# Kernel tuning notes

Hardware: AMD Instinct MI355X
Metric: run time of the kernel (lower is better)

## Reference

```python
import jax, jax.numpy as jnp
import numpy as np

N = 50000
E = 800000
IN_C = 128
OUT_C = 64   # per-head dim C == out_channels (concat=False)
HEADS = 4
FFN_H = 256
SQRT_HALF = 0.70710678
LN_EPS = 1e-7


def setup_inputs() -> dict:
    key = jax.random.key(0)
    ks = jax.random.split(key, 16)
    s = 0.05
    return {
        "x": jax.random.normal(ks[0], (N, IN_C), jnp.float32),
        "edge_index": jax.random.randint(ks[1], (2, E), 0, N, jnp.int64),
        # GATv2 params
        "Wl": jax.random.normal(ks[2], (HEADS * OUT_C, IN_C), jnp.float32) * s,
        "Wr": jax.random.normal(ks[3], (HEADS * OUT_C, IN_C), jnp.float32) * s,
        "att": jax.random.normal(ks[4], (HEADS, OUT_C), jnp.float32) * s,
        "bias": jax.random.normal(ks[5], (OUT_C,), jnp.float32) * s,
        # block linears
        "W_affn1": jax.random.normal(ks[6], (OUT_C, IN_C), jnp.float32) * s,
        "b_affn1": jnp.zeros((OUT_C,), jnp.float32),
        "W_affn2": jax.random.normal(ks[7], (OUT_C, OUT_C), jnp.float32) * s,
        "b_affn2": jnp.zeros((OUT_C,), jnp.float32),
        # layernorms
        "g1": jnp.ones((IN_C,), jnp.float32),
        "beta1": jnp.zeros((IN_C,), jnp.float32),
        "g2": jnp.ones((OUT_C,), jnp.float32),
        "beta2": jnp.zeros((OUT_C,), jnp.float32),
        # FFN: out_channels -> 256 -> out_channels
        "W1": jax.random.normal(ks[8], (FFN_H, OUT_C), jnp.float32) * s,
        "b1": jnp.zeros((FFN_H,), jnp.float32),
        "W2": jax.random.normal(ks[9], (OUT_C, FFN_H), jnp.float32) * s,
        "b2": jnp.zeros((OUT_C,), jnp.float32),
    }


def _ln(v, g, b):
    m = jnp.mean(v, axis=-1, keepdims=True)
    var = jnp.var(v, axis=-1, keepdims=True)
    return (v - m) * jax.lax.rsqrt(var + LN_EPS) * g + b


def reference(x, edge_index, Wl, Wr, att, bias, W_affn1, b_affn1,
              W_affn2, b_affn2, g1, beta1, g2, beta2, W1, b1, W2, b2):
    n = x.shape[0]
    H, C = att.shape
    dst = edge_index[0]
    src = edge_index[1]

    x_res = x @ W_affn1.T + b_affn1            # (N, OUT_C)
    h = _ln(x, g1, beta1)                      # (N, IN_C)

    # GATv2 attention (concat=False, no self loops)
    x_l = (h @ Wl.T).reshape(n, H, C)
    x_r = (h @ Wr.T).reshape(n, H, C)
    x_j = x_r[src]                             # (E, H, C)
    e = jax.nn.leaky_relu(x_l[dst] + x_j, 0.2) # (E, H, C)
    logits = jnp.einsum('ehc,hc->eh', e, att)  # (E, H)

    # segment softmax over destination nodes (per head)
    mx = jax.ops.segment_max(logits, dst, num_segments=n)
    ex = jnp.exp(logits - mx[dst])
    den = jax.ops.segment_sum(ex, dst, num_segments=n)
    alpha = ex / (den[dst] + 1e-16)            # (E, H)

    agg = jnp.zeros((n, H, C), x.dtype).at[dst].add(x_j * alpha[..., None])
    attn_out = jnp.mean(agg, axis=1) + bias    # (N, OUT_C)

    out = SQRT_HALF * attn_out + SQRT_HALF * x_res

    # FFN half of the block (pre-LN, matching the attention half's structure)
    h2 = _ln(out, g2, beta2)
    f = jax.nn.relu(h2 @ W1.T + b1) @ W2.T + b2
    res2 = out @ W_affn2.T + b_affn2
    return SQRT_HALF * f + SQRT_HALF * res2
```

## Files before the change

kernel.cpp:

```cpp
#include <hip/hip_runtime.h>
#include <hip/hip_bf16.h>
#include <hip/hip_fp16.h>
#include <math.h>


#define SQRT_HALF 0.70710678f
#define LN_EPS 1e-7f

typedef __attribute__((ext_vector_type(8))) short bf16x8;
typedef __attribute__((ext_vector_type(4))) float f32x4;
typedef _Float16 f16x2 __attribute__((ext_vector_type(2)));

__device__ __forceinline__ float wave_reduce_sum64(float v) {
  #pragma unroll
  for (int m = 1; m < 64; m <<= 1) v += __shfl_xor(v, m, 64);
  return v;
}
__device__ __forceinline__ unsigned short f2bf_bits(float f) {
  __hip_bfloat16 b = __float2bfloat16(f);
  return *reinterpret_cast<unsigned short*>(&b);
}
__device__ __forceinline__ unsigned int pack2bf(float lo, float hi) {
  return (unsigned int)f2bf_bits(lo) | ((unsigned int)f2bf_bits(hi) << 16);
}
__device__ __forceinline__ __half2 u2h(unsigned int u) {
  union { unsigned int u; __half2 h; } c; c.u = u; return c.h;
}
__device__ __forceinline__ __half2 h2abs(__half2 v) {
  union { __half2 h; unsigned int u; } c; c.h = v;
  c.u &= 0x7fff7fffu;
  return c.h;
}
__device__ __forceinline__ f16x2 h2f(__half2 h) {
  union { __half2 h; f16x2 f; } c; c.h = h; return c.f;
}
__device__ __forceinline__ __half2 shflx_h2(__half2 v, int m) {
  union { unsigned int u; __half2 h; } c; c.h = v;
  c.u = (unsigned int)__shfl_xor((int)c.u, m, 64);
  return c.h;
}
__device__ __forceinline__ float dpp_xor1_add(float p) {
  int t = __builtin_amdgcn_update_dpp(0, __float_as_int(p), 0xB1, 0xf, 0xf, true);
  return p + __int_as_float(t);
}
__device__ __forceinline__ float dpp_xor2_add(float p) {
  int t = __builtin_amdgcn_update_dpp(0, __float_as_int(p), 0x4E, 0xf, 0xf, true);
  return p + __int_as_float(t);
}

__global__ __launch_bounds__(256) void phase0(
    const float* __restrict__ x, const float* __restrict__ g1,
    const float* __restrict__ beta1, __hip_bfloat16* __restrict__ h,
    __hip_bfloat16* __restrict__ xbf,
    const float* __restrict__ wl, const float* __restrict__ wr,
    const float* __restrict__ wa1, const float* __restrict__ w1,
    const float* __restrict__ w2, const float* __restrict__ wa2,
    const float* __restrict__ b2c, const float* __restrict__ ba2,
    const float* __restrict__ att,
    __hip_bfloat16* __restrict__ wcat, __hip_bfloat16* __restrict__ wa1b,
    __hip_bfloat16* __restrict__ w1b, __hip_bfloat16* __restrict__ w2b,
    __hip_bfloat16* __restrict__ wa2b, __half* __restrict__ att2,
    float* __restrict__ biasc,
    const int* __restrict__ ei, int* __restrict__ cursorE,
    unsigned short* __restrict__ ell,
    int E_, int n, int gLN, int gW) {
  int bx = blockIdx.x;
  if (bx < gLN) {
    int node = bx * 4 + (threadIdx.x >> 6);
    if (node >= n) return;
    int lane = threadIdx.x & 63;
    const float* xr = x + (size_t)node * 128;
    float a = xr[lane], c = xr[lane + 64];
    float s1 = wave_reduce_sum64(a + c) * (1.f / 128.f);
    float s2 = wave_reduce_sum64(a * a + c * c) * (1.f / 128.f);
    float inv = rsqrtf(s2 - s1 * s1 + LN_EPS);
    __hip_bfloat16* hr = h + (size_t)node * 128;
    hr[lane]      = __float2bfloat16((a - s1) * inv * g1[lane] + beta1[lane]);
    hr[lane + 64] =
        __float2bfloat16((c - s1) * inv * g1[lane + 64] + beta1[lane + 64]);
    __hip_bfloat16* xbr = xbf + (size_t)node * 128;
    xbr[lane]      = __float2bfloat16(a);
    xbr[lane + 64] = __float2bfloat16(c);
  } else if (bx < gLN + gW) {
    int i = (bx - gLN) * 256 + threadIdx.x;
    if (i < 65536) {
      wcat[i] = __float2bfloat16(i < 32768 ? wl[i] : wr[i - 32768]);
    } else if (i < 73728) {
      int j = i - 65536; wa1b[j] = __float2bfloat16(wa1[j]);
    } else if (i < 90112) {
      int j = i - 73728; w1b[j] = __float2bfloat16(w1[j]);
    } else if (i < 106496) {
      int j = i - 90112; w2b[j] = __float2bfloat16(w2[j]);
    } else if (i < 110592) {
      int j = i - 106496; wa2b[j] = __float2bfloat16(wa2[j]);
    } else if (i < 110848) {
      int j = i - 110592; att2[j] = __float2half(att[j]);
    } else if (i < 110912) {
      int j = i - 110848; biasc[j] = SQRT_HALF * (b2c[j] + ba2[j]);
    }
  } else {
    int e = (bx - gLN - gW) * 256 + threadIdx.x;
    if (e < E_) {
      int dst = ei[e], src = ei[E_ + e];
      int pos = atomicAdd(&cursorE[dst << 4], 1);
      if (pos < 64) ell[((size_t)dst << 6) + pos] = (unsigned short)src;
    }
  }
}

__global__ __launch_bounds__(256) void mfma_pre(
    const short* __restrict__ h, const short* __restrict__ xbf,
    const short* __restrict__ wcat, const short* __restrict__ wa1b,
    const float* __restrict__ ba1, __half* __restrict__ xlxr,
    float* __restrict__ xres, int n, int ntiles) {
  int tid = threadIdx.x;
  int wv = tid >> 6, l = tid & 63;
  int lane_m = l & 15, kg = l >> 4;
  if (blockIdx.y < 4) {
    int bn = blockIdx.y * 128;
    bf16x8 wf[4][8];
    const short* wp = wcat + (size_t)(bn + lane_m) * 128 + kg * 8;
    #pragma unroll
    for (int ks = 0; ks < 4; ++ks)
      #pragma unroll
      for (int ct = 0; ct < 8; ++ct)
        wf[ks][ct] = *(const bf16x8*)(wp + (size_t)ct * 16 * 128 + ks * 32);
    for (int t = blockIdx.x; t < ntiles; t += gridDim.x) {
      int node = t * 64 + wv * 16 + lane_m;
      int nodec = node < n ? node : n - 1;
      const short* ap = h + (size_t)nodec * 128 + kg * 8;
      f32x4 acc[8] = {};
      #pragma unroll
      for (int ks = 0; ks < 4; ++ks) {
        bf16x8 af = *(const bf16x8*)(ap + ks * 32);
        #pragma unroll
        for (int ct = 0; ct < 8; ++ct)
          acc[ct] = __builtin_amdgcn_mfma_f32_16x16x32_bf16(
              wf[ks][ct], af, acc[ct], 0, 0, 0);
      }
      if (node < n) {
        #pragma unroll
        for (int ct = 0; ct < 8; ++ct) {
          int col = bn + ct * 16 + kg * 4;
          ushort4 s;
          s.x = __half_as_ushort(__float2half(acc[ct][0]));
          s.y = __half_as_ushort(__float2half(acc[ct][1]));
          s.z = __half_as_ushort(__float2half(acc[ct][2]));
          s.w = __half_as_ushort(__float2half(acc[ct][3]));
          *(ushort4*)((unsigned short*)xlxr + (size_t)node * 512 + col) = s;
        }
      }
    }
  } else {
    bf16x8 wf[4][4];
    const short* wp = wa1b + (size_t)lane_m * 128 + kg * 8;
    #pragma unroll
    for (int ks = 0; ks < 4; ++ks)
      #pragma unroll
      for (int ct = 0; ct < 4; ++ct)
        wf[ks][ct] = *(const bf16x8*)(wp + (size_t)ct * 16 * 128 + ks * 32);
    float4 bias4[4];
    #pragma unroll
    for (int ct = 0; ct < 4; ++ct)
      bias4[ct] = *(const float4*)(ba1 + ct * 16 + kg * 4);
    for (int t = blockIdx.x; t < ntiles; t += gridDim.x) {
      int node = t * 64 + wv * 16 + lane_m;
      int nodec = node < n ? node : n - 1;
      const short* ap = xbf + (size_t)nodec * 128 + kg * 8;
      f32x4 acc[4] = {};
      #pragma unroll
      for (int ks = 0; ks < 4; ++ks) {
        bf16x8 af = *(const bf16x8*)(ap + ks * 32);
        #pragma unroll
        for (int ct = 0; ct < 4; ++ct)
          acc[ct] = __builtin_amdgcn_mfma_f32_16x16x32_bf16(
              wf[ks][ct], af, acc[ct], 0, 0, 0);
      }
      if (node < n) {
        #pragma unroll
        for (int ct = 0; ct < 4; ++ct) {
          int col = ct * 16 + kg * 4;
          *(float4*)(xres + (size_t)node * 64 + col) = make_float4(
              acc[ct][0] + ((const float*)&bias4[ct])[0],
              acc[ct][1] + ((const float*)&bias4[ct])[1],
              acc[ct][2] + ((const float*)&bias4[ct])[2],
              acc[ct][3] + ((const float*)&bias4[ct])[3]);
        }
      }
    }
  }
}

__global__ __launch_bounds__(256) void fused_edge_kernel(
    const int* __restrict__ cursorE, const unsigned short* __restrict__ ell,
    const __half* __restrict__ xlxr,
    const __half* __restrict__ att2, const float* __restrict__ xres,
    const float* __restrict__ bias, const float* __restrict__ g2,
    const float* __restrict__ b2, __hip_bfloat16* __restrict__ outb,
    __hip_bfloat16* __restrict__ h2, int n) {
  int node = blockIdx.x * 4 + (threadIdx.x >> 6);
  if (node >= n) return;
  int lane = threadIdx.x & 63;
  int half_ = lane >> 5;
  int hl = lane & 31;
  int q = hl & 7;
  int off8 = (hl >> 3) * 64 + q * 8;
  uint4 va = *(const uint4*)(xlxr + (size_t)node * 512 + off8);
  __half2 xa2[4] = {u2h(va.x), u2h(va.y), u2h(va.z), u2h(va.w)};
  uint4 vt = *(const uint4*)(att2 + off8);
  const __half2 c06 = __float2half2_rn(0.6f);
  const __half2 c04 = __float2half2_rn(0.4f);
  __half2 at6[4], at4[4];
  #pragma unroll
  for (int c = 0; c < 4; ++c) {
    __half2 a = u2h(((const unsigned int*)&vt)[c]);
    at6[c] = __hmul2(c06, a);
    at4[c] = __hmul2(c04, a);
  }
  int d = cursorE[node << 4];
  d = d < 64 ? d : 64;
  float den = 0.f;
  __half2 ac2[4] = {__float2half2_rn(0.f), __float2half2_rn(0.f),
                    __float2half2_rn(0.f), __float2half2_rn(0.f)};
  if (d > 0) {
    int dm1 = d - 1;
    int dpairs = d >> 1;
    const __half* xrbase = xlxr + 256 + off8;
    int myidx = (int)ell[((size_t)node << 6) + (lane <= dm1 ? lane : dm1)];
    int srcA = __shfl(myidx, half_ <= dm1 ? half_ : dm1, 64);
    int srcB = __shfl(myidx, 2 + half_ <= dm1 ? 2 + half_ : dm1, 64);
    uint4 vbA = *(const uint4*)(xrbase + (size_t)srcA * 512);
    uint4 vbB = *(const uint4*)(xrbase + (size_t)srcB * 512);
    #pragma unroll 2
    for (int k = 0; k < dpairs; ++k) {
      int jC = 2 * k + 4 + half_;
      jC = jC <= dm1 ? jC : dm1;
      int srcC = __shfl(myidx, jC, 64);
      uint4 vbC = *(const uint4*)(xrbase + (size_t)srcC * 512);
      __half2 xb2[4] = {u2h(vbA.x), u2h(vbA.y), u2h(vbA.z), u2h(vbA.w)};
      float p = 0.f;
      #pragma unroll
      for (int c = 0; c < 4; ++c) {
        __half2 s = __hadd2(xa2[c], xb2[c]);
        p = __builtin_amdgcn_fdot2(h2f(at6[c]), h2f(s), p, false);
        p = __builtin_amdgcn_fdot2(h2f(at4[c]), h2f(h2abs(s)), p, false);
      }
      p = dpp_xor1_add(p);
      p = dpp_xor2_add(p);
      p += __shfl_xor(p, 4, 64);
      float ex = __expf(p);
      den += ex;
      __half2 ex2 = __float2half2_rn(ex);
      #pragma unroll
      for (int c = 0; c < 4; ++c) ac2[c] = __hfma2(ex2, xb2[c], ac2[c]);
      vbA = vbB; vbB = vbC;
    }
    if (d & 1) {
      __half2 xb2[4] = {u2h(vbA.x), u2h(vbA.y), u2h(vbA.z), u2h(vbA.w)};
      float p = 0.f;
      #pragma unroll
      for (int c = 0; c < 4; ++c) {
        __half2 s = __hadd2(xa2[c], xb2[c]);
        p = __builtin_amdgcn_fdot2(h2f(at6[c]), h2f(s), p, false);
        p = __builtin_amdgcn_fdot2(h2f(at4[c]), h2f(h2abs(s)), p, false);
      }
      p = dpp_xor1_add(p);
      p = dpp_xor2_add(p);
      p += __shfl_xor(p, 4, 64);
      float ex = (half_ == 0) ? __expf(p) : 0.f;
      den += ex;
      __half2 ex2 = __float2half2_rn(ex);
      #pragma unroll
      for (int c = 0; c < 4; ++c) ac2[c] = __hfma2(ex2, xb2[c], ac2[c]);
    }
  }
  #pragma unroll
  for (int c = 0; c < 4; ++c) ac2[c] = __hadd2(ac2[c], shflx_h2(ac2[c], 32));
  den += __shfl_xor(den, 32, 64);
  float inv = 1.f / (den + 1e-16f);
  __half2 inv2 = __float2half2_rn(inv);
  #pragma unroll
  for (int c = 0; c < 4; ++c) {
    __half2 a = __hmul2(ac2[c], inv2);
    a = __hadd2(a, shflx_h2(a, 8));
    a = __hadd2(a, shflx_h2(a, 16));
    ac2[c] = a;
  }
  float acf[8];
  #pragma unroll
  for (int c = 0; c < 4; ++c) {
    acf[2 * c]     = __low2float(ac2[c]);
    acf[2 * c + 1] = __high2float(ac2[c]);
  }
  float o[8];
  {
    float4 bi0 = *(const float4*)(bias + q * 8);
    float4 bi1 = *(const float4*)(bias + q * 8 + 4);
    float4 xr0 = *(const float4*)(xres + (size_t)node * 64 + q * 8);
    float4 xr1 = *(const float4*)(xres + (size_t)node * 64 + q * 8 + 4);
    float bi[8] = {bi0.x, bi0.y, bi0.z, bi0.w, bi1.x, bi1.y, bi1.z, bi1.w};
    float xr[8] = {xr0.x, xr0.y, xr0.z, xr0.w, xr1.x, xr1.y, xr1.z, xr1.w};
    #pragma unroll
    for (int c = 0; c < 8; ++c)
      o[c] = SQRT_HALF * (acf[c] * 0.25f + bi[c] + xr[c]);
  }
  float s1 = 0.f, s2 = 0.f;
  #pragma unroll
  for (int c = 0; c < 8; ++c) { s1 += o[c]; s2 += o[c] * o[c]; }
  s1 = dpp_xor1_add(s1); s2 = dpp_xor1_add(s2);
  s1 = dpp_xor2_add(s1); s2 = dpp_xor2_add(s2);
  s1 += __shfl_xor(s1, 4, 64); s2 += __shfl_xor(s2, 4, 64);
  float mean = s1 * (1.f / 64.f);
  float var = s2 * (1.f / 64.f) - mean * mean;
  float rinv = rsqrtf(var + LN_EPS);
  if (lane < 8) {
    float4 g0 = *(const float4*)(g2 + q * 8);
    float4 g1v = *(const float4*)(g2 + q * 8 + 4);
    float4 e0 = *(const float4*)(b2 + q * 8);
    float4 e1 = *(const float4*)(b2 + q * 8 + 4);
    float gg[8] = {g0.x, g0.y, g0.z, g0.w, g1v.x, g1v.y, g1v.z, g1v.w};
    float ee[8] = {e0.x, e0.y, e0.z, e0.w, e1.x, e1.y, e1.z, e1.w};
    uint4 ov, hv;
    ov.x = pack2bf(o[0], o[1]); ov.y = pack2bf(o[2], o[3]);
    ov.z = pack2bf(o[4], o[5]); ov.w = pack2bf(o[6], o[7]);
    float t[8];
    #pragma unroll
    for (int c = 0; c < 8; ++c)
      t[c] = (o[c] - mean) * rinv * gg[c] + ee[c];
    hv.x = pack2bf(t[0], t[1]); hv.y = pack2bf(t[2], t[3]);
    hv.z = pack2bf(t[4], t[5]); hv.w = pack2bf(t[6], t[7]);
    *(uint4*)((unsigned short*)outb + (size_t)node * 64 + q * 8) = ov;
    *(uint4*)((unsigned short*)h2 + (size_t)node * 64 + q * 8) = hv;
  }
}

__global__ __launch_bounds__(256) void ffn_fused(
    const __hip_bfloat16* __restrict__ h2, const __hip_bfloat16* __restrict__ outb,
    const __hip_bfloat16* __restrict__ w1b, const __hip_bfloat16* __restrict__ w2b,
    const __hip_bfloat16* __restrict__ wa2b, const float* __restrict__ b1,
    const float* __restrict__ biasc, float* __restrict__ out,
    int n, int ntiles) {
  __shared__ unsigned short lds[4][16][280];
  int tid = threadIdx.x;
  int wv = tid >> 6, l = tid & 63;
  int lane_m = l & 15, kg = l >> 4;
  bf16x8 wf1[2][16];
  #pragma unroll
  for (int ks = 0; ks < 2; ++ks)
    #pragma unroll
    for (int ct = 0; ct < 16; ++ct)
      wf1[ks][ct] = *(const bf16x8*)(
          (const short*)w1b + (size_t)(ct * 16 + lane_m) * 64 + ks * 32 + kg * 8);
  for (int t = blockIdx.x; t < ntiles; t += gridDim.x) {
    int node = t * 64 + wv * 16 + lane_m;
    int nodec = node < n ? node : n - 1;
    const short* hp = (const short*)h2 + (size_t)nodec * 64 + kg * 8;
    bf16x8 af1[2];
    af1[0] = *(const bf16x8*)(hp);
    af1[1] = *(const bf16x8*)(hp + 32);
    f32x4 acc1[16] = {};
    #pragma unroll
    for (int ks = 0; ks < 2; ++ks)
      #pragma unroll
      for (int ct = 0; ct < 16; ++ct)
        acc1[ct] = __builtin_amdgcn_mfma_f32_16x16x32_bf16(
            wf1[ks][ct], af1[ks], acc1[ct], 0, 0, 0);
    #pragma unroll
    for (int ct = 0; ct < 16; ++ct) {
      float4 bb = *(const float4*)(b1 + ct * 16 + kg * 4);
      ushort4 s;
      s.x = f2bf_bits(fmaxf(acc1[ct][0] + bb.x, 0.f));
      s.y = f2bf_bits(fmaxf(acc1[ct][1] + bb.y, 0.f));
      s.z = f2bf_bits(fmaxf(acc1[ct][2] + bb.z, 0.f));
      s.w = f2bf_bits(fmaxf(acc1[ct][3] + bb.w, 0.f));
      *(ushort4*)&lds[wv][lane_m][ct * 16 + kg * 4] = s;
    }
    f32x4 acc2[4] = {};
    #pragma unroll
    for (int ks = 0; ks < 8; ++ks) {
      bf16x8 af2 = *(const bf16x8*)&lds[wv][lane_m][ks * 32 + kg * 8];
      #pragma unroll
      for (int ct = 0; ct < 4; ++ct) {
        bf16x8 wf2 = *(const bf16x8*)(
            (const short*)w2b + (size_t)(ct * 16 + lane_m) * 256 + ks * 32 + kg * 8);
        acc2[ct] = __builtin_amdgcn_mfma_f32_16x16x32_bf16(
            wf2, af2, acc2[ct], 0, 0, 0);
      }
    }
    const short* op = (const short*)outb + (size_t)nodec * 64 + kg * 8;
    #pragma unroll
    for (int ks = 0; ks < 2; ++ks) {
      bf16x8 afo = *(const bf16x8*)(op + ks * 32);
      #pragma unroll
      for (int ct = 0; ct < 4; ++ct) {
        bf16x8 wfo = *(const bf16x8*)(
            (const short*)wa2b + (size_t)(ct * 16 + lane_m) * 64 + ks * 32 + kg * 8);
        acc2[ct] = __builtin_amdgcn_mfma_f32_16x16x32_bf16(
            wfo, afo, acc2[ct], 0, 0, 0);
      }
    }
    if (node < n) {
      #pragma unroll
      for (int ct = 0; ct < 4; ++ct) {
        float4 bc = *(const float4*)(biasc + ct * 16 + kg * 4);
        float4 v = make_float4(SQRT_HALF * acc2[ct][0] + bc.x,
                               SQRT_HALF * acc2[ct][1] + bc.y,
                               SQRT_HALF * acc2[ct][2] + bc.z,
                               SQRT_HALF * acc2[ct][3] + bc.w);
        *(float4*)(out + (size_t)node * 64 + ct * 16 + kg * 4) = v;
      }
    }
  }
}

extern "C" void kernel_launch(void* const* d_in, const int* in_sizes, int n_in,
                              void* d_out, int out_size, void* d_ws,
                              size_t ws_size, hipStream_t stream) {
  const float* x       = (const float*)d_in[0];
  const int*   ei      = (const int*)d_in[1];
  const float* Wl      = (const float*)d_in[2];
  const float* Wr      = (const float*)d_in[3];
  const float* att     = (const float*)d_in[4];
  const float* bias    = (const float*)d_in[5];
  const float* W_affn1 = (const float*)d_in[6];
  const float* b_affn1 = (const float*)d_in[7];
  const float* W_affn2 = (const float*)d_in[8];
  const float* b_affn2 = (const float*)d_in[9];
  const float* g1      = (const float*)d_in[10];
  const float* beta1   = (const float*)d_in[11];
  const float* g2      = (const float*)d_in[12];
  const float* beta2   = (const float*)d_in[13];
  const float* W1      = (const float*)d_in[14];
  const float* b1      = (const float*)d_in[15];
  const float* W2      = (const float*)d_in[16];
  const float* b2      = (const float*)d_in[17];
  int n  = in_sizes[0] / 128;
  int E_ = in_sizes[1] / 2;

  float* ws = (float*)d_ws;
  size_t o_xlxr = 0;
  size_t o_h    = o_xlxr + (size_t)n * 256;
  size_t o_xbf  = o_h + (size_t)n * 64;
  size_t o_xres = o_xbf + (size_t)n * 64;
  size_t o_h2   = o_xres + (size_t)n * 64;
  size_t o_outb = o_h2 + (size_t)n * 32;
  size_t o_w    = o_outb + (size_t)n * 32;
  __half* xlxr         = (__half*)(ws + o_xlxr);
  __hip_bfloat16* h    = (__hip_bfloat16*)(ws + o_h);
  __hip_bfloat16* xbf  = (__hip_bfloat16*)(ws + o_xbf);
  float* xres          = ws + o_xres;
  __hip_bfloat16* h2   = (__hip_bfloat16*)(ws + o_h2);
  __hip_bfloat16* outb = (__hip_bfloat16*)(ws + o_outb);
  __hip_bfloat16* wcat = (__hip_bfloat16*)(ws + o_w);
  __hip_bfloat16* wa1b = (__hip_bfloat16*)(ws + o_w + 32768);
  __hip_bfloat16* w1b  = (__hip_bfloat16*)(ws + o_w + 36864);
  __hip_bfloat16* w2b  = (__hip_bfloat16*)(ws + o_w + 45056);
  __hip_bfloat16* wa2b = (__hip_bfloat16*)(ws + o_w + 53248);
  __half* att2         = (__half*)(ws + o_w + 55296);
  float* biasc         = ws + o_w + 55424;
  size_t o_int = o_w + 55488;
  int* iw        = (int*)(ws + o_int);
  int* cursorE   = iw;
  unsigned short* ell =
      (unsigned short*)(iw + (size_t)n * 16);

  int ntiles = (n + 63) / 64;
  int gLN = (n + 3) / 4;
  int gW = (110912 + 255) / 256;
  int gH = (E_ + 255) / 256;

  (void)hipMemsetAsync(cursorE, 0, (size_t)n * 16 * 4, stream);

  phase0<<<gLN + gW + gH, 256, 0, stream>>>(
      x, g1, beta1, h, xbf, Wl, Wr, W_affn1, W1, W2, W_affn2, b2, b_affn2,
      att, wcat, wa1b, w1b, w2b, wa2b, att2, biasc, ei, cursorE, ell,
      E_, n, gLN, gW);

  mfma_pre<<<dim3(128, 5), 256, 0, stream>>>(
      (const short*)h, (const short*)xbf, (const short*)wcat,
      (const short*)wa1b, b_affn1, xlxr, xres, n, ntiles);

  fused_edge_kernel<<<(n + 3) / 4, 256, 0, stream>>>(
      cursorE, ell, xlxr, att2, xres, bias, g2, beta2, outb, h2, n);

  ffn_fused<<<ntiles, 256, 0, stream>>>(
      h2, outb, w1b, w2b, wa2b, b1, biasc, (float*)d_out, n, ntiles);
}
```

Baseline: 219.8 us.

## Move edge bucketing into GEMM kernel with split front/back cursors

Drops the memset and zeroes the per-node cursors inside phase0. The ELL bucketing of edges moves into a sixth y-slice of mfma_pre, so the scatter overlaps the projection GEMMs, with a 4-way unrolled grid-stride loop. Odd and even threads use two separate cursor arrays, filling slots from the front and from the back, which halves atomic contention per destination. The edge kernel merges the two counts and maps slot indices. The cost is extra cursor memory and per-lane index remapping. Overflow beyond 64 neighbours is now split differently between the two halves.

```diff
diff --git a/kernel.cpp b/kernel.cpp
--- a/kernel.cpp
+++ b/kernel.cpp
@@ -61,9 +61,8 @@
     __hip_bfloat16* __restrict__ w1b, __hip_bfloat16* __restrict__ w2b,
     __hip_bfloat16* __restrict__ wa2b, __half* __restrict__ att2,
     float* __restrict__ biasc,
-    const int* __restrict__ ei, int* __restrict__ cursorE,
-    unsigned short* __restrict__ ell,
-    int E_, int n, int gLN, int gW) {
+    int* __restrict__ cursorA, int* __restrict__ cursorB,
+    int n, int gLN, int gW) {
   int bx = blockIdx.x;
   if (bx < gLN) {
     int node = bx * 4 + (threadIdx.x >> 6);
@@ -99,11 +98,10 @@
       int j = i - 110848; biasc[j] = SQRT_HALF * (b2c[j] + ba2[j]);
     }
   } else {
-    int e = (bx - gLN - gW) * 256 + threadIdx.x;
-    if (e < E_) {
-      int dst = ei[e], src = ei[E_ + e];
-      int pos = atomicAdd(&cursorE[dst << 4], 1);
-      if (pos < 64) ell[((size_t)dst << 6) + pos] = (unsigned short)src;
+    int i = (bx - gLN - gW) * 256 + threadIdx.x;
+    if (i < n) {
+      cursorA[i << 4] = 0;
+      cursorB[i << 4] = 0;
     }
   }
 }
@@ -112,7 +110,9 @@
     const short* __restrict__ h, const short* __restrict__ xbf,
     const short* __restrict__ wcat, const short* __restrict__ wa1b,
     const float* __restrict__ ba1, __half* __restrict__ xlxr,
-    float* __restrict__ xres, int n, int ntiles) {
+    float* __restrict__ xres, const int* __restrict__ ei,
+    int* __restrict__ cursorA, int* __restrict__ cursorB,
+    unsigned short* __restrict__ ell, int E_, int n, int ntiles) {
   int tid = threadIdx.x;
   int wv = tid >> 6, l = tid & 63;
   int lane_m = l & 15, kg = l >> 4;
@@ -151,7 +151,7 @@
         }
       }
     }
-  } else {
+  } else if (blockIdx.y == 4) {
     bf16x8 wf[4][4];
     const short* wp = wa1b + (size_t)lane_m * 128 + kg * 8;
     #pragma unroll
@@ -188,11 +188,36 @@
         }
       }
     }
+  } else {
+    int stride = gridDim.x * 256;
+    bool back = (tid & 1) != 0;
+    int* cur = back ? cursorB : cursorA;
+    int e = blockIdx.x * 256 + tid;
+    for (; e + 3 * stride < E_; e += 4 * stride) {
+      int d0 = ei[e], d1 = ei[e + stride];
+      int d2 = ei[e + 2 * stride], d3 = ei[e + 3 * stride];
+      int s0 = ei[E_ + e], s1 = ei[E_ + e + stride];
+      int s2 = ei[E_ + e + 2 * stride], s3 = ei[E_ + e + 3 * stride];
+      int p0 = atomicAdd(&cur[d0 << 4], 1);
+      int p1 = atomicAdd(&cur[d1 << 4], 1);
+      int p2 = atomicAdd(&cur[d2 << 4], 1);
+      int p3 = atomicAdd(&cur[d3 << 4], 1);
+      if (p0 < 64) ell[((size_t)d0 << 6) + (back ? 63 - p0 : p0)] = (unsigned short)s0;
+      if (p1 < 64) ell[((size_t)d1 << 6) + (back ? 63 - p1 : p1)] = (unsigned short)s1;
+      if (p2 < 64) ell[((size_t)d2 << 6) + (back ? 63 - p2 : p2)] = (unsigned short)s2;
+      if (p3 < 64) ell[((size_t)d3 << 6) + (back ? 63 - p3 : p3)] = (unsigned short)s3;
+    }
+    for (; e < E_; e += stride) {
+      int dst = ei[e], src = ei[E_ + e];
+      int pos = atomicAdd(&cur[dst << 4], 1);
+      if (pos < 64) ell[((size_t)dst << 6) + (back ? 63 - pos : pos)] = (unsigned short)src;
+    }
   }
 }
 
 __global__ __launch_bounds__(256) void fused_edge_kernel(
-    const int* __restrict__ cursorE, const unsigned short* __restrict__ ell,
+    const int* __restrict__ cursorA, const int* __restrict__ cursorB,
+    const unsigned short* __restrict__ ell,
     const __half* __restrict__ xlxr,
     const __half* __restrict__ att2, const float* __restrict__ xres,
     const float* __restrict__ bias, const float* __restrict__ g2,
@@ -217,8 +242,11 @@
     at6[c] = __hmul2(c06, a);
     at4[c] = __hmul2(c04, a);
   }
-  int d = cursorE[node << 4];
-  d = d < 64 ? d : 64;
+  int dA = cursorA[node << 4];
+  int dB = cursorB[node << 4];
+  dA = dA < 64 ? dA : 64;
+  dB = dB < 64 - dA ? dB : 64 - dA;
+  int d = dA + dB;
   float den = 0.f;
   __half2 ac2[4] = {__float2half2_rn(0.f), __float2half2_rn(0.f),
                     __float2half2_rn(0.f), __float2half2_rn(0.f)};
@@ -226,7 +254,9 @@
     int dm1 = d - 1;
     int dpairs = d >> 1;
     const __half* xrbase = xlxr + 256 + off8;
-    int myidx = (int)ell[((size_t)node << 6) + (lane <= dm1 ? lane : dm1)];
+    int j0 = lane <= dm1 ? lane : dm1;
+    int slot = j0 < dA ? j0 : 63 - (j0 - dA);
+    int myidx = (int)ell[((size_t)node << 6) + slot];
     int srcA = __shfl(myidx, half_ <= dm1 ? half_ : dm1, 64);
     int srcB = __shfl(myidx, 2 + half_ <= dm1 ? 2 + half_ : dm1, 64);
     uint4 vbA = *(const uint4*)(xrbase + (size_t)srcA * 512);
@@ -460,28 +490,28 @@
   float* biasc         = ws + o_w + 55424;
   size_t o_int = o_w + 55488;
   int* iw        = (int*)(ws + o_int);
-  int* cursorE   = iw;
+  int* cursorA   = iw;
+  int* cursorB   = iw + (size_t)n * 16;
   unsigned short* ell =
-      (unsigned short*)(iw + (size_t)n * 16);
+      (unsigned short*)(iw + (size_t)n * 32);
 
   int ntiles = (n + 63) / 64;
   int gLN = (n + 3) / 4;
   int gW = (110912 + 255) / 256;
-  int gH = (E_ + 255) / 256;
-
-  (void)hipMemsetAsync(cursorE, 0, (size_t)n * 16 * 4, stream);
-
-  phase0<<<gLN + gW + gH, 256, 0, stream>>>(
+  int gZ = (n + 255) / 256;
+
+  phase0<<<gLN + gW + gZ, 256, 0, stream>>>(
       x, g1, beta1, h, xbf, Wl, Wr, W_affn1, W1, W2, W_affn2, b2, b_affn2,
-      att, wcat, wa1b, w1b, w2b, wa2b, att2, biasc, ei, cursorE, ell,
-      E_, n, gLN, gW);
-
-  mfma_pre<<<dim3(128, 5), 256, 0, stream>>>(
+      att, wcat, wa1b, w1b, w2b, wa2b, att2, biasc, cursorA, cursorB,
+      n, gLN, gW);
+
+  mfma_pre<<<dim3(128, 6), 256, 0, stream>>>(
       (const short*)h, (const short*)xbf, (const short*)wcat,
-      (const short*)wa1b, b_affn1, xlxr, xres, n, ntiles);
+      (const short*)wa1b, b_affn1, xlxr, xres, ei, cursorA, cursorB, ell,
+      E_, n, ntiles);
 
   fused_edge_kernel<<<(n + 3) / 4, 256, 0, stream>>>(
-      cursorE, ell, xlxr, att2, xres, bias, g2, beta2, outb, h2, n);
+      cursorA, cursorB, ell, xlxr, att2, xres, bias, g2, beta2, outb, h2, n);
 
   ffn_fused<<<ntiles, 256, 0, stream>>>(
       h2, outb, w1b, w2b, wa2b, b1, biasc, (float*)d_out, n, ntiles);
```

New measurement: 197.2 us. 1.11x faster.

## Fuse LayerNorm, weight conversion and ELL build into the projection GEMM kernel

Applied to the files above, without the earlier changes.

Merges the phase0 and mfma_pre kernels into one. Each GEMM tile now computes LayerNorm on the fly from fp32 x and converts Wl/Wr/W_affn1 to bf16 in registers, so the bf16 h/xbf intermediates and the converted weight buffers are no longer written or read. The ELL adjacency build and the small weight conversions run in a sixth grid row using a grid-stride loop unrolled by four, overlapping with the GEMM blocks. This removes one launch and the intermediate round trips. In exchange, each of the four xl/xr column blocks redundantly recomputes LayerNorm from fp32 x, and the atomics-heavy ELL work now runs on fewer blocks.

```diff
diff --git a/kernel.cpp b/kernel.cpp
--- a/kernel.cpp
+++ b/kernel.cpp
@@ -11,11 +11,6 @@
 typedef __attribute__((ext_vector_type(4))) float f32x4;
 typedef _Float16 f16x2 __attribute__((ext_vector_type(2)));
 
-__device__ __forceinline__ float wave_reduce_sum64(float v) {
-  #pragma unroll
-  for (int m = 1; m < 64; m <<= 1) v += __shfl_xor(v, m, 64);
-  return v;
-}
 __device__ __forceinline__ unsigned short f2bf_bits(float f) {
   __hip_bfloat16 b = __float2bfloat16(f);
   return *reinterpret_cast<unsigned short*>(&b);
@@ -47,97 +42,93 @@
   int t = __builtin_amdgcn_update_dpp(0, __float_as_int(p), 0x4E, 0xf, 0xf, true);
   return p + __int_as_float(t);
 }
-
-__global__ __launch_bounds__(256) void phase0(
+__device__ __forceinline__ bf16x8 cvt8(float4 a0, float4 a1) {
+  bf16x8 v;
+  v[0] = (short)f2bf_bits(a0.x); v[1] = (short)f2bf_bits(a0.y);
+  v[2] = (short)f2bf_bits(a0.z); v[3] = (short)f2bf_bits(a0.w);
+  v[4] = (short)f2bf_bits(a1.x); v[5] = (short)f2bf_bits(a1.y);
+  v[6] = (short)f2bf_bits(a1.z); v[7] = (short)f2bf_bits(a1.w);
+  return v;
+}
+
+__global__ __launch_bounds__(256) void fused_pre(
     const float* __restrict__ x, const float* __restrict__ g1,
-    const float* __restrict__ beta1, __hip_bfloat16* __restrict__ h,
-    __hip_bfloat16* __restrict__ xbf,
+    const float* __restrict__ beta1,
     const float* __restrict__ wl, const float* __restrict__ wr,
-    const float* __restrict__ wa1, const float* __restrict__ w1,
+    const float* __restrict__ wa1, const float* __restrict__ ba1,
+    const float* __restrict__ att, const float* __restrict__ w1,
     const float* __restrict__ w2, const float* __restrict__ wa2,
     const float* __restrict__ b2c, const float* __restrict__ ba2,
-    const float* __restrict__ att,
-    __hip_bfloat16* __restrict__ wcat, __hip_bfloat16* __restrict__ wa1b,
+    __half* __restrict__ xlxr, float* __restrict__ xres,
     __hip_bfloat16* __restrict__ w1b, __hip_bfloat16* __restrict__ w2b,
     __hip_bfloat16* __restrict__ wa2b, __half* __restrict__ att2,
     float* __restrict__ biasc,
     const int* __restrict__ ei, int* __restrict__ cursorE,
     unsigned short* __restrict__ ell,
-    int E_, int n, int gLN, int gW) {
-  int bx = blockIdx.x;
-  if (bx < gLN) {
-    int node = bx * 4 + (threadIdx.x >> 6);
-    if (node >= n) return;
-    int lane = threadIdx.x & 63;
-    const float* xr = x + (size_t)node * 128;
-    float a = xr[lane], c = xr[lane + 64];
-    float s1 = wave_reduce_sum64(a + c) * (1.f / 128.f);
-    float s2 = wave_reduce_sum64(a * a + c * c) * (1.f / 128.f);
-    float inv = rsqrtf(s2 - s1 * s1 + LN_EPS);
-    __hip_bfloat16* hr = h + (size_t)node * 128;
-    hr[lane]      = __float2bfloat16((a - s1) * inv * g1[lane] + beta1[lane]);
-    hr[lane + 64] =
-        __float2bfloat16((c - s1) * inv * g1[lane + 64] + beta1[lane + 64]);
-    __hip_bfloat16* xbr = xbf + (size_t)node * 128;
-    xbr[lane]      = __float2bfloat16(a);
-    xbr[lane + 64] = __float2bfloat16(c);
-  } else if (bx < gLN + gW) {
-    int i = (bx - gLN) * 256 + threadIdx.x;
-    if (i < 65536) {
-      wcat[i] = __float2bfloat16(i < 32768 ? wl[i] : wr[i - 32768]);
-    } else if (i < 73728) {
-      int j = i - 65536; wa1b[j] = __float2bfloat16(wa1[j]);
-    } else if (i < 90112) {
-      int j = i - 73728; w1b[j] = __float2bfloat16(w1[j]);
-    } else if (i < 106496) {
-      int j = i - 90112; w2b[j] = __float2bfloat16(w2[j]);
-    } else if (i < 110592) {
-      int j = i - 106496; wa2b[j] = __float2bfloat16(wa2[j]);
-    } else if (i < 110848) {
-      int j = i - 110592; att2[j] = __float2half(att[j]);
-    } else if (i < 110912) {
-      int j = i - 110848; biasc[j] = SQRT_HALF * (b2c[j] + ba2[j]);
-    }
-  } else {
-    int e = (bx - gLN - gW) * 256 + threadIdx.x;
-    if (e < E_) {
-      int dst = ei[e], src = ei[E_ + e];
-      int pos = atomicAdd(&cursorE[dst << 4], 1);
-      if (pos < 64) ell[((size_t)dst << 6) + pos] = (unsigned short)src;
-    }
-  }
-}
-
-__global__ __launch_bounds__(256) void mfma_pre(
-    const short* __restrict__ h, const short* __restrict__ xbf,
-    const short* __restrict__ wcat, const short* __restrict__ wa1b,
-    const float* __restrict__ ba1, __half* __restrict__ xlxr,
-    float* __restrict__ xres, int n, int ntiles) {
+    int E_, int n, int ntiles) {
   int tid = threadIdx.x;
   int wv = tid >> 6, l = tid & 63;
   int lane_m = l & 15, kg = l >> 4;
   if (blockIdx.y < 4) {
     int bn = blockIdx.y * 128;
+    const float* wsrc = (bn < 256) ? (wl + (size_t)bn * 128)
+                                   : (wr + (size_t)(bn - 256) * 128);
     bf16x8 wf[4][8];
-    const short* wp = wcat + (size_t)(bn + lane_m) * 128 + kg * 8;
-    #pragma unroll
-    for (int ks = 0; ks < 4; ++ks)
-      #pragma unroll
-      for (int ct = 0; ct < 8; ++ct)
-        wf[ks][ct] = *(const bf16x8*)(wp + (size_t)ct * 16 * 128 + ks * 32);
+    #pragma unroll
+    for (int ct = 0; ct < 8; ++ct) {
+      const float* wrow = wsrc + (size_t)(ct * 16 + lane_m) * 128 + kg * 8;
+      #pragma unroll
+      for (int ks = 0; ks < 4; ++ks) {
+        float4 a0 = *(const float4*)(wrow + ks * 32);
+        float4 a1 = *(const float4*)(wrow + ks * 32 + 4);
+        wf[ks][ct] = cvt8(a0, a1);
+      }
+    }
     for (int t = blockIdx.x; t < ntiles; t += gridDim.x) {
       int node = t * 64 + wv * 16 + lane_m;
       int nodec = node < n ? node : n - 1;
-      const short* ap = h + (size_t)nodec * 128 + kg * 8;
+      const float* xrow = x + (size_t)nodec * 128 + kg * 8;
+      float4 xr0[4], xr1[4];
+      float s1 = 0.f, s2 = 0.f;
+      #pragma unroll
+      for (int ks = 0; ks < 4; ++ks) {
+        xr0[ks] = *(const float4*)(xrow + ks * 32);
+        xr1[ks] = *(const float4*)(xrow + ks * 32 + 4);
+        s1 += xr0[ks].x + xr0[ks].y + xr0[ks].z + xr0[ks].w +
+              xr1[ks].x + xr1[ks].y + xr1[ks].z + xr1[ks].w;
+        s2 += xr0[ks].x * xr0[ks].x + xr0[ks].y * xr0[ks].y +
+              xr0[ks].z * xr0[ks].z + xr0[ks].w * xr0[ks].w +
+              xr1[ks].x * xr1[ks].x + xr1[ks].y * xr1[ks].y +
+              xr1[ks].z * xr1[ks].z + xr1[ks].w * xr1[ks].w;
+      }
+      s1 += __shfl_xor(s1, 16, 64); s1 += __shfl_xor(s1, 32, 64);
+      s2 += __shfl_xor(s2, 16, 64); s2 += __shfl_xor(s2, 32, 64);
+      float mean = s1 * (1.f / 128.f);
+      float inv = rsqrtf(s2 * (1.f / 128.f) - mean * mean + LN_EPS);
+      bf16x8 af[4];
+      #pragma unroll
+      for (int ks = 0; ks < 4; ++ks) {
+        const float* gp = g1 + kg * 8 + ks * 32;
+        const float* bp = beta1 + kg * 8 + ks * 32;
+        float4 g0 = *(const float4*)(gp), g1v = *(const float4*)(gp + 4);
+        float4 e0 = *(const float4*)(bp), e1 = *(const float4*)(bp + 4);
+        float4 n0 = make_float4((xr0[ks].x - mean) * inv * g0.x + e0.x,
+                                (xr0[ks].y - mean) * inv * g0.y + e0.y,
+                                (xr0[ks].z - mean) * inv * g0.z + e0.z,
+                                (xr0[ks].w - mean) * inv * g0.w + e0.w);
+        float4 n1 = make_float4((xr1[ks].x - mean) * inv * g1v.x + e1.x,
+                                (xr1[ks].y - mean) * inv * g1v.y + e1.y,
+                                (xr1[ks].z - mean) * inv * g1v.z + e1.z,
+                                (xr1[ks].w - mean) * inv * g1v.w + e1.w);
+        af[ks] = cvt8(n0, n1);
+      }
       f32x4 acc[8] = {};
       #pragma unroll
-      for (int ks = 0; ks < 4; ++ks) {
-        bf16x8 af = *(const bf16x8*)(ap + ks * 32);
+      for (int ks = 0; ks < 4; ++ks)
         #pragma unroll
         for (int ct = 0; ct < 8; ++ct)
           acc[ct] = __builtin_amdgcn_mfma_f32_16x16x32_bf16(
-              wf[ks][ct], af, acc[ct], 0, 0, 0);
-      }
+              wf[ks][ct], af[ks], acc[ct], 0, 0, 0);
       if (node < n) {
         #pragma unroll
         for (int ct = 0; ct < 8; ++ct) {
@@ -151,14 +142,18 @@
         }
       }
     }
-  } else {
+  } else if (blockIdx.y == 4) {
     bf16x8 wf[4][4];
-    const short* wp = wa1b + (size_t)lane_m * 128 + kg * 8;
-    #pragma unroll
-    for (int ks = 0; ks < 4; ++ks)
-      #pragma unroll
-      for (int ct = 0; ct < 4; ++ct)
-        wf[ks][ct] = *(const bf16x8*)(wp + (size_t)ct * 16 * 128 + ks * 32);
+    #pragma unroll
+    for (int ct = 0; ct < 4; ++ct) {
+      const float* wrow = wa1 + (size_t)(ct * 16 + lane_m) * 128 + kg * 8;
+      #pragma unroll
+      for (int ks = 0; ks < 4; ++ks) {
+        float4 a0 = *(const float4*)(wrow + ks * 32);
+        float4 a1 = *(const float4*)(wrow + ks * 32 + 4);
+        wf[ks][ct] = cvt8(a0, a1);
+      }
+    }
     float4 bias4[4];
     #pragma unroll
     for (int ct = 0; ct < 4; ++ct)
@@ -166,16 +161,21 @@
     for (int t = blockIdx.x; t < ntiles; t += gridDim.x) {
       int node = t * 64 + wv * 16 + lane_m;
       int nodec = node < n ? node : n - 1;
-      const short* ap = xbf + (size_t)nodec * 128 + kg * 8;
+      const float* xrow = x + (size_t)nodec * 128 + kg * 8;
+      bf16x8 af[4];
+      #pragma unroll
+      for (int ks = 0; ks < 4; ++ks) {
+        float4 a0 = *(const float4*)(xrow + ks * 32);
+        float4 a1 = *(const float4*)(xrow + ks * 32 + 4);
+        af[ks] = cvt8(a0, a1);
+      }
       f32x4 acc[4] = {};
       #pragma unroll
-      for (int ks = 0; ks < 4; ++ks) {
-        bf16x8 af = *(const bf16x8*)(ap + ks * 32);
+      for (int ks = 0; ks < 4; ++ks)
         #pragma unroll
         for (int ct = 0; ct < 4; ++ct)
           acc[ct] = __builtin_amdgcn_mfma_f32_16x16x32_bf16(
-              wf[ks][ct], af, acc[ct], 0, 0, 0);
-      }
+              wf[ks][ct], af[ks], acc[ct], 0, 0, 0);
       if (node < n) {
         #pragma unroll
         for (int ct = 0; ct < 4; ++ct) {
@@ -187,6 +187,40 @@
               acc[ct][3] + ((const float*)&bias4[ct])[3]);
         }
       }
+    }
+  } else {
+    int gid = blockIdx.x * 256 + tid;
+    if (gid < 16384) {
+      w1b[gid] = __float2bfloat16(w1[gid]);
+    } else if (gid < 32768) {
+      int j = gid - 16384; w2b[j] = __float2bfloat16(w2[j]);
+    } else if (gid < 36864) {
+      int j = gid - 32768; wa2b[j] = __float2bfloat16(wa2[j]);
+    } else if (gid < 37120) {
+      int j = gid - 36864; att2[j] = __float2half(att[j]);
+    } else if (gid < 37184) {
+      int j = gid - 37120; biasc[j] = SQRT_HALF * (b2c[j] + ba2[j]);
+    }
+    int stride = gridDim.x * 256;
+    int e = blockIdx.x * 256 + tid;
+    for (; e + 3 * stride < E_; e += 4 * stride) {
+      int d0 = ei[e], d1 = ei[e + stride];
+      int d2 = ei[e + 2 * stride], d3 = ei[e + 3 * stride];
+      int s0 = ei[E_ + e], s1 = ei[E_ + e + stride];
+      int s2 = ei[E_ + e + 2 * stride], s3 = ei[E_ + e + 3 * stride];
+      int p0 = atomicAdd(&cursorE[d0 << 4], 1);
+      int p1 = atomicAdd(&cursorE[d1 << 4], 1);
+      int p2 = atomicAdd(&cursorE[d2 << 4], 1);
+      int p3 = atomicAdd(&cursorE[d3 << 4], 1);
+      if (p0 < 64) ell[((size_t)d0 << 6) + p0] = (unsigned short)s0;
+      if (p1 < 64) ell[((size_t)d1 << 6) + p1] = (unsigned short)s1;
+      if (p2 < 64) ell[((size_t)d2 << 6) + p2] = (unsigned short)s2;
+      if (p3 < 64) ell[((size_t)d3 << 6) + p3] = (unsigned short)s3;
+    }
+    for (; e < E_; e += stride) {
+      int dst = ei[e], src = ei[E_ + e];
+      int pos = atomicAdd(&cursorE[dst << 4], 1);
+      if (pos < 64) ell[((size_t)dst << 6) + pos] = (unsigned short)src;
     }
   }
 }
@@ -439,46 +473,33 @@
 
   float* ws = (float*)d_ws;
   size_t o_xlxr = 0;
-  size_t o_h    = o_xlxr + (size_t)n * 256;
-  size_t o_xbf  = o_h + (size_t)n * 64;
-  size_t o_xres = o_xbf + (size_t)n * 64;
+  size_t o_xres = o_xlxr + (size_t)n * 256;
   size_t o_h2   = o_xres + (size_t)n * 64;
   size_t o_outb = o_h2 + (size_t)n * 32;
   size_t o_w    = o_outb + (size_t)n * 32;
   __half* xlxr         = (__half*)(ws + o_xlxr);
-  __hip_bfloat16* h    = (__hip_bfloat16*)(ws + o_h);
-  __hip_bfloat16* xbf  = (__hip_bfloat16*)(ws + o_xbf);
   float* xres          = ws + o_xres;
   __hip_bfloat16* h2   = (__hip_bfloat16*)(ws + o_h2);
   __hip_bfloat16* outb = (__hip_bfloat16*)(ws + o_outb);
-  __hip_bfloat16* wcat = (__hip_bfloat16*)(ws + o_w);
-  __hip_bfloat16* wa1b = (__hip_bfloat16*)(ws + o_w + 32768);
-  __hip_bfloat16* w1b  = (__hip_bfloat16*)(ws + o_w + 36864);
-  __hip_bfloat16* w2b  = (__hip_bfloat16*)(ws + o_w + 45056);
-  __hip_bfloat16* wa2b = (__hip_bfloat16*)(ws + o_w + 53248);
-  __half* att2         = (__half*)(ws + o_w + 55296);
-  float* biasc         = ws + o_w + 55424;
-  size_t o_int = o_w + 55488;
+  __hip_bfloat16* w1b  = (__hip_bfloat16*)(ws + o_w);
+  __hip_bfloat16* w2b  = (__hip_bfloat16*)(ws + o_w + 8192);
+  __hip_bfloat16* wa2b = (__hip_bfloat16*)(ws + o_w + 16384);
+  __half* att2         = (__half*)(ws + o_w + 18432);
+  float* biasc         = ws + o_w + 18560;
+  size_t o_int = o_w + 18624;
   int* iw        = (int*)(ws + o_int);
   int* cursorE   = iw;
   unsigned short* ell =
       (unsigned short*)(iw + (size_t)n * 16);
 
   int ntiles = (n + 63) / 64;
-  int gLN = (n + 3) / 4;
-  int gW = (110912 + 255) / 256;
-  int gH = (E_ + 255) / 256;
 
   (void)hipMemsetAsync(cursorE, 0, (size_t)n * 16 * 4, stream);
 
-  phase0<<<gLN + gW + gH, 256, 0, stream>>>(
-      x, g1, beta1, h, xbf, Wl, Wr, W_affn1, W1, W2, W_affn2, b2, b_affn2,
-      att, wcat, wa1b, w1b, w2b, wa2b, att2, biasc, ei, cursorE, ell,
-      E_, n, gLN, gW);
-
-  mfma_pre<<<dim3(128, 5), 256, 0, stream>>>(
-      (const short*)h, (const short*)xbf, (const short*)wcat,
-      (const short*)wa1b, b_affn1, xlxr, xres, n, ntiles);
+  fused_pre<<<dim3(192, 6), 256, 0, stream>>>(
+      x, g1, beta1, Wl, Wr, W_affn1, b_affn1, att, W1, W2, W_affn2,
+      b2, b_affn2, xlxr, xres, w1b, w2b, wa2b, att2, biasc,
+      ei, cursorE, ell, E_, n, ntiles);
 
   fused_edge_kernel<<<(n + 3) / 4, 256, 0, stream>>>(
       cursorE, ell, xlxr, att2, xres, bias, g2, beta2, outb, h2, n);
```

Result: faster. 200.6 us (-8.7%).

## Build ELL adjacency via chunked LDS histograms and scan instead of global atomics

Applied to the files above, without the earlier changes.

Replaces the global-atomic ELL construction with a two-pass, counting-sort-style build. Each of 128 edge chunks first histograms destination degrees into packed 8-bit LDS bins, a scan kernel turns these into per-chunk offsets and a degree per node, and the scatter pass then runs as a sixth slice of the mfma_pre grid. This removes the memset and the contended global atomicAdd per edge, and lets the fill overlap with the GEMM blocks. In exchange it adds a kernel launch, a second read of edge_index, 51 KB of LDS in prep and mfma_pre that may reduce occupancy of the GEMM blocks, and 8-bit counters that overflow for in-degree of 256 or more.

```diff
diff --git a/kernel.cpp b/kernel.cpp
--- a/kernel.cpp
+++ b/kernel.cpp
@@ -48,7 +48,10 @@
   return p + __int_as_float(t);
 }
 
-__global__ __launch_bounds__(256) void phase0(
+#define NCHUNK 128
+#define WMAX 12800
+
+__global__ __launch_bounds__(256) void prep_kernel(
     const float* __restrict__ x, const float* __restrict__ g1,
     const float* __restrict__ beta1, __hip_bfloat16* __restrict__ h,
     __hip_bfloat16* __restrict__ xbf,
@@ -61,14 +64,14 @@
     __hip_bfloat16* __restrict__ w1b, __hip_bfloat16* __restrict__ w2b,
     __hip_bfloat16* __restrict__ wa2b, __half* __restrict__ att2,
     float* __restrict__ biasc,
-    const int* __restrict__ ei, int* __restrict__ cursorE,
-    unsigned short* __restrict__ ell,
-    int E_, int n, int gLN, int gW) {
-  int bx = blockIdx.x;
+    const int* __restrict__ ei, unsigned int* __restrict__ counts,
+    int E_, int n, int W, int S, int gLN) {
+  __shared__ unsigned int bins[WMAX];
+  int bx = blockIdx.x, tid = threadIdx.x;
   if (bx < gLN) {
-    int node = bx * 4 + (threadIdx.x >> 6);
+    int node = bx * 4 + (tid >> 6);
     if (node >= n) return;
-    int lane = threadIdx.x & 63;
+    int lane = tid & 63;
     const float* xr = x + (size_t)node * 128;
     float a = xr[lane], c = xr[lane + 64];
     float s1 = wave_reduce_sum64(a + c) * (1.f / 128.f);
@@ -81,38 +84,77 @@
     __hip_bfloat16* xbr = xbf + (size_t)node * 128;
     xbr[lane]      = __float2bfloat16(a);
     xbr[lane + 64] = __float2bfloat16(c);
-  } else if (bx < gLN + gW) {
-    int i = (bx - gLN) * 256 + threadIdx.x;
-    if (i < 65536) {
-      wcat[i] = __float2bfloat16(i < 32768 ? wl[i] : wr[i - 32768]);
-    } else if (i < 73728) {
-      int j = i - 65536; wa1b[j] = __float2bfloat16(wa1[j]);
-    } else if (i < 90112) {
-      int j = i - 73728; w1b[j] = __float2bfloat16(w1[j]);
-    } else if (i < 106496) {
-      int j = i - 90112; w2b[j] = __float2bfloat16(w2[j]);
-    } else if (i < 110592) {
-      int j = i - 106496; wa2b[j] = __float2bfloat16(wa2[j]);
-    } else if (i < 110848) {
-      int j = i - 110592; att2[j] = __float2half(att[j]);
-    } else if (i < 110912) {
-      int j = i - 110848; biasc[j] = SQRT_HALF * (b2c[j] + ba2[j]);
-    }
+  } else if (bx < gLN + NCHUNK) {
+    int c = bx - gLN;
+    for (int i = tid; i < W; i += 256) bins[i] = 0u;
+    __syncthreads();
+    int e0 = c * S, e1 = c * S + S;
+    if (e1 > E_) e1 = E_;
+    for (int e = e0 + tid; e < e1; e += 256) {
+      int dst = ei[e];
+      atomicAdd(&bins[dst >> 2], 1u << ((dst & 3) * 8));
+    }
+    __syncthreads();
+    unsigned int* crow = counts + (size_t)c * W;
+    for (int i = tid; i < W; i += 256) crow[i] = bins[i];
   } else {
-    int e = (bx - gLN - gW) * 256 + threadIdx.x;
-    if (e < E_) {
-      int dst = ei[e], src = ei[E_ + e];
-      int pos = atomicAdd(&cursorE[dst << 4], 1);
-      if (pos < 64) ell[((size_t)dst << 6) + pos] = (unsigned short)src;
-    }
-  }
+    int gid = (bx - gLN - NCHUNK) * 256 + tid;
+    for (int i = gid; i < 110912; i += 64 * 256) {
+      if (i < 65536) {
+        wcat[i] = __float2bfloat16(i < 32768 ? wl[i] : wr[i - 32768]);
+      } else if (i < 73728) {
+        int j = i - 65536; wa1b[j] = __float2bfloat16(wa1[j]);
+      } else if (i < 90112) {
+        int j = i - 73728; w1b[j] = __float2bfloat16(w1[j]);
+      } else if (i < 106496) {
+        int j = i - 90112; w2b[j] = __float2bfloat16(w2[j]);
+      } else if (i < 110592) {
+        int j = i - 106496; wa2b[j] = __float2bfloat16(wa2[j]);
+      } else if (i < 110848) {
+        int j = i - 110592; att2[j] = __float2half(att[j]);
+      } else {
+        int j = i - 110848; biasc[j] = SQRT_HALF * (b2c[j] + ba2[j]);
+      }
+    }
+  }
+}
+
+__global__ __launch_bounds__(256) void scan_kernel(
+    unsigned int* __restrict__ counts, unsigned int* __restrict__ degw,
+    int W) {
+  int gid = blockIdx.x * 256 + threadIdx.x;
+  int w = gid >> 3, g = gid & 7;
+  if (w >= W) return;
+  unsigned int v[16];
+  unsigned int s = 0;
+  #pragma unroll
+  for (int i = 0; i < 16; ++i) {
+    v[i] = counts[(size_t)(g * 16 + i) * W + w];
+    s += v[i];
+  }
+  unsigned int run = s;
+  #pragma unroll
+  for (int off = 1; off < 8; off <<= 1) {
+    unsigned int u = __shfl_up(run, off, 64);
+    if (g >= off) run += u;
+  }
+  unsigned int base = run - s;
+  #pragma unroll
+  for (int i = 0; i < 16; ++i) {
+    counts[(size_t)(g * 16 + i) * W + w] = base;
+    base += v[i];
+  }
+  if (g == 7) degw[w] = base;
 }
 
 __global__ __launch_bounds__(256) void mfma_pre(
     const short* __restrict__ h, const short* __restrict__ xbf,
     const short* __restrict__ wcat, const short* __restrict__ wa1b,
     const float* __restrict__ ba1, __half* __restrict__ xlxr,
-    float* __restrict__ xres, int n, int ntiles) {
+    float* __restrict__ xres, const int* __restrict__ ei,
+    const unsigned int* __restrict__ counts, unsigned short* __restrict__ ell,
+    int E_, int n, int W, int S, int ntiles) {
+  __shared__ unsigned int bins[WMAX];
   int tid = threadIdx.x;
   int wv = tid >> 6, l = tid & 63;
   int lane_m = l & 15, kg = l >> 4;
@@ -151,7 +193,7 @@
         }
       }
     }
-  } else {
+  } else if (blockIdx.y == 4) {
     bf16x8 wf[4][4];
     const short* wp = wa1b + (size_t)lane_m * 128 + kg * 8;
     #pragma unroll
@@ -188,11 +230,28 @@
         }
       }
     }
+  } else {
+    int c = blockIdx.x;
+    if (c >= NCHUNK) return;
+    for (int i = tid; i < W; i += 256) bins[i] = 0u;
+    __syncthreads();
+    int e0 = c * S, e1 = c * S + S;
+    if (e1 > E_) e1 = E_;
+    const unsigned int* cbase = counts + (size_t)c * W;
+    for (int e = e0 + tid; e < e1; e += 256) {
+      int dst = ei[e], src = ei[E_ + e];
+      int sh = (dst & 3) * 8;
+      unsigned int old = atomicAdd(&bins[dst >> 2], 1u << sh);
+      int local = (int)((old >> sh) & 0xffu);
+      int base = (int)((cbase[dst >> 2] >> sh) & 0xffu);
+      int slot = base + local;
+      if (slot < 64) ell[((size_t)dst << 6) + slot] = (unsigned short)src;
+    }
   }
 }
 
 __global__ __launch_bounds__(256) void fused_edge_kernel(
-    const int* __restrict__ cursorE, const unsigned short* __restrict__ ell,
+    const unsigned int* __restrict__ degw, const unsigned short* __restrict__ ell,
     const __half* __restrict__ xlxr,
     const __half* __restrict__ att2, const float* __restrict__ xres,
     const float* __restrict__ bias, const float* __restrict__ g2,
@@ -217,7 +276,7 @@
     at6[c] = __hmul2(c06, a);
     at4[c] = __hmul2(c04, a);
   }
-  int d = cursorE[node << 4];
+  int d = (int)((degw[node >> 2] >> ((node & 3) * 8)) & 0xffu);
   d = d < 64 ? d : 64;
   float den = 0.f;
   __half2 ac2[4] = {__float2half2_rn(0.f), __float2half2_rn(0.f),
@@ -437,6 +496,11 @@
   int n  = in_sizes[0] / 128;
   int E_ = in_sizes[1] / 2;
 
+  int W = (n + 3) >> 2;
+  int S = (E_ + NCHUNK - 1) / NCHUNK;
+  int ntiles = (n + 63) / 64;
+  int gLN = (n + 3) / 4;
+
   float* ws = (float*)d_ws;
   size_t o_xlxr = 0;
   size_t o_h    = o_xlxr + (size_t)n * 256;
@@ -458,30 +522,25 @@
   __hip_bfloat16* wa2b = (__hip_bfloat16*)(ws + o_w + 53248);
   __half* att2         = (__half*)(ws + o_w + 55296);
   float* biasc         = ws + o_w + 55424;
-  size_t o_int = o_w + 55488;
-  int* iw        = (int*)(ws + o_int);
-  int* cursorE   = iw;
-  unsigned short* ell =
-      (unsigned short*)(iw + (size_t)n * 16);
-
-  int ntiles = (n + 63) / 64;
-  int gLN = (n + 3) / 4;
-  int gW = (110912 + 255) / 256;
-  int gH = (E_ + 255) / 256;
-
-  (void)hipMemsetAsync(cursorE, 0, (size_t)n * 16 * 4, stream);
-
-  phase0<<<gLN + gW + gH, 256, 0, stream>>>(
+  size_t o_cnt = o_w + 55488;
+  unsigned int* counts = (unsigned int*)(ws + o_cnt);
+  unsigned int* degw   = counts + (size_t)NCHUNK * W;
+  unsigned short* ell  = (unsigned short*)(degw + W);
+
+  prep_kernel<<<gLN + NCHUNK + 64, 256, 0, stream>>>(
       x, g1, beta1, h, xbf, Wl, Wr, W_affn1, W1, W2, W_affn2, b2, b_affn2,
-      att, wcat, wa1b, w1b, w2b, wa2b, att2, biasc, ei, cursorE, ell,
-      E_, n, gLN, gW);
-
-  mfma_pre<<<dim3(128, 5), 256, 0, stream>>>(
+      att, wcat, wa1b, w1b, w2b, wa2b, att2, biasc, ei, counts,
+      E_, n, W, S, gLN);
+
+  scan_kernel<<<(W * 8 + 255) / 256, 256, 0, stream>>>(counts, degw, W);
+
+  mfma_pre<<<dim3(NCHUNK, 6), 256, 0, stream>>>(
       (const short*)h, (const short*)xbf, (const short*)wcat,
-      (const short*)wa1b, b_affn1, xlxr, xres, n, ntiles);
+      (const short*)wa1b, b_affn1, xlxr, xres, ei, counts, ell,
+      E_, n, W, S, ntiles);
 
   fused_edge_kernel<<<(n + 3) / 4, 256, 0, stream>>>(
-      cursorE, ell, xlxr, att2, xres, bias, g2, beta2, outb, h2, n);
+      degw, ell, xlxr, att2, xres, bias, g2, beta2, outb, h2, n);
 
   ffn_fused<<<ntiles, 256, 0, stream>>>(
       h2, outb, w1b, w2b, wa2b, b1, biasc, (float*)d_out, n, ntiles);
```

After: 199.2 us. 1.1x faster.
